# Optimization experiments

Hardware: AMD Instinct MI355X
Metric: run time of the kernel (lower is better)

## Reference

```python
import jax, jax.numpy as jnp
import numpy as np

B, N, D = 8, 1024, 768
H = 12
HD = D // H


def setup_inputs() -> dict:
    key = jax.random.key(0)
    ks = jax.random.split(key, 9)
    s = 1.0 / np.sqrt(D)
    return {
        "x": jax.random.normal(ks[0], (B, N, D), dtype=jnp.float32),
        "Wq": jax.random.normal(ks[1], (D, D), dtype=jnp.float32) * s,
        "bq": jax.random.normal(ks[2], (D,), dtype=jnp.float32) * 0.02,
        "Wk": jax.random.normal(ks[3], (D, D), dtype=jnp.float32) * s,
        "bk": jax.random.normal(ks[4], (D,), dtype=jnp.float32) * 0.02,
        "Wv": jax.random.normal(ks[5], (D, D), dtype=jnp.float32) * s,
        "bv": jax.random.normal(ks[6], (D,), dtype=jnp.float32) * 0.02,
        "Wo": jax.random.normal(ks[7], (D, D), dtype=jnp.float32) * s,
        "bo": jax.random.normal(ks[8], (D,), dtype=jnp.float32) * 0.02,
    }


def _softmax_one(x):
    # quiet softmax: exp(x - max) / (1 + sum exp(x - max))
    x = x - jnp.max(x, axis=-1, keepdims=True)
    ex = jnp.exp(x)
    return ex / (1.0 + jnp.sum(ex, axis=-1, keepdims=True))


def reference(x, Wq, bq, Wk, bk, Wv, bv, Wo, bo):
    q = x @ Wq + bq  # [B,N,D]
    k = x @ Wk + bk
    v = x @ Wv + bv
    # split heads -> [B,H,N,HD]
    qs = q.reshape(B, N, H, HD).transpose(0, 2, 1, 3)
    ks = k.reshape(B, N, H, HD).transpose(0, 2, 1, 3)
    vs = v.reshape(B, N, H, HD).transpose(0, 2, 1, 3)
    scores = jnp.einsum("bhqd,bhkd->bhqk", qs, ks) / np.sqrt(HD)
    attn = _softmax_one(scores)  # quiet_attention=True
    ctx = jnp.einsum("bhqk,bhkd->bhqd", attn, vs)
    ctx = ctx.transpose(0, 2, 1, 3).reshape(B, N, D)
    return ctx @ Wo + bo
```

## Files before the change

kernel.cpp:

```cpp
#include <hip/hip_runtime.h>
#include <cstdint>

#define DEV __device__ __forceinline__

typedef __bf16 bf16x4 __attribute__((ext_vector_type(4)));
typedef __bf16 bf16x8 __attribute__((ext_vector_type(8)));
typedef float  floatx4 __attribute__((ext_vector_type(4)));
typedef float  floatx16 __attribute__((ext_vector_type(16)));
typedef unsigned uint4v __attribute__((ext_vector_type(4)));

constexpr int BB = 8, NSEQ = 1024, DMODEL = 768, NH = 12, HD = 64;
constexpr int MTOK = BB * NSEQ;
constexpr int NQKV = 3 * DMODEL;
constexpr float CS = 0.18033688011112042f;

DEV void async_copy16(void* lds, const void* g) {
    __builtin_amdgcn_global_load_lds(
        (__attribute__((address_space(1))) void*)(const_cast<void*>(g)),
        (__attribute__((address_space(3))) void*)lds,
        16, 0, 0);
}

DEV floatx4 mfma16x32(bf16x8 a, bf16x8 b, floatx4 c) {
    return __builtin_amdgcn_mfma_f32_16x16x32_bf16(a, b, c, 0, 0, 0);
}
DEV floatx16 mfma32x16(bf16x8 a, bf16x8 b, floatx16 c) {
    return __builtin_amdgcn_mfma_f32_32x32x16_bf16(a, b, c, 0, 0, 0);
}
DEV unsigned cvtpk(float a, float b) {
    unsigned r;
    asm("v_cvt_pk_bf16_f32 %0, %1, %2" : "=v"(r) : "v"(a), "v"(b));
    return r;
}
DEV void swap32(unsigned& x, unsigned& y) {
    asm("v_permlane32_swap_b32 %0, %1" : "+v"(x), "+v"(y));
}


__global__ __launch_bounds__(256) void k_prep(const float* __restrict__ x,
                                              __bf16* __restrict__ xb,
                                              const float* __restrict__ Wq,
                                              const float* __restrict__ Wk,
                                              const float* __restrict__ Wv,
                                              const float* __restrict__ Wo,
                                              __bf16* __restrict__ wtqkv,
                                              __bf16* __restrict__ wto,
                                              const float* __restrict__ bq,
                                              const float* __restrict__ bk,
                                              const float* __restrict__ bv,
                                              float* __restrict__ bqkv) {
    __shared__ float tile[32][33];
    int bid = blockIdx.x, t = threadIdx.x;
    if (bid < 6144) {
        int i = (bid * 256 + t) * 4;
        float4 v = *(const float4*)(x + i);
        bf16x4 o;
        o[0] = (__bf16)v.x; o[1] = (__bf16)v.y; o[2] = (__bf16)v.z; o[3] = (__bf16)v.w;
        *(bf16x4*)(xb + i) = o;
    } else if (bid < 8448) {
        int idx = bid - 6144;
        int z = idx / 576, rem = idx % 576;
        int k0 = (rem % 24) * 32, n0 = (rem / 24) * 32;
        const float* W = (z == 0) ? Wq : (z == 1) ? Wk : (z == 2) ? Wv : Wo;
        int tx = t & 31, ty = t >> 5;
#pragma unroll
        for (int p = 0; p < 4; p++)
            tile[ty + 8 * p][tx] = W[(size_t)(k0 + ty + 8 * p) * 768 + n0 + tx];
        __syncthreads();
        __bf16* out = (z < 3) ? (wtqkv + (size_t)z * 768 * 768) : wto;
#pragma unroll
        for (int p = 0; p < 4; p++)
            out[(size_t)(n0 + ty + 8 * p) * 768 + k0 + tx] = (__bf16)tile[tx][ty + 8 * p];
    } else {
        int i = (bid - 8448) * 256 + t;
        if (i < 768) bqkv[i] = bq[i];
        else if (i < 1536) bqkv[i] = bk[i - 768];
        else bqkv[i] = bv[i - 1536];
    }
}

__global__ __launch_bounds__(256) void k_qkv(const __bf16* __restrict__ A,
                                             const __bf16* __restrict__ Bt,
                                             const float* __restrict__ bias,
                                             __bf16* __restrict__ qfb,
                                             __bf16* __restrict__ kfb,
                                             __bf16* __restrict__ vfb) {
    constexpr int SLOT = 16384;
    __shared__ __align__(16) __bf16 lds[2 * SLOT];
    int t = threadIdx.x, lane = t & 63, w = t >> 6;
    int quad = lane >> 4, n16 = lane & 15;
    int wm = w & 1, wn = w >> 1;
    int m0 = blockIdx.x * 128, n0 = blockIdx.y * 128;
    floatx4 acc[4][4] = {};

    auto stage_tile = [&](__bf16* slot, int k0) {
        __bf16* As_ = slot;
        __bf16* Bs_ = slot + 8192;
#pragma unroll
        for (int i = 0; i < 4; i++) {
            int off = t + i * 256;
            int row = off >> 3, pc = off & 7;
            int c = pc ^ (row & 7);
            async_copy16(&As_[row * 64 + pc * 8],
                         &A[(size_t)(m0 + row) * 768 + k0 + c * 8]);
        }
#pragma unroll
        for (int i = 0; i < 4; i++) {
            int off = t + i * 256;
            int row = off >> 3, pc = off & 7;
            int c = pc ^ (row & 7);
            async_copy16(&Bs_[row * 64 + pc * 8],
                         &Bt[(size_t)(n0 + row) * 768 + k0 + c * 8]);
        }
    };

    stage_tile(lds, 0);

#pragma unroll
    for (int kt = 0; kt < 12; kt++) {
        __bf16* As_ = lds + (kt & 1) * SLOT;
        __bf16* Bs_ = As_ + 8192;

        if (kt + 1 < 12) stage_tile(lds + ((kt + 1) & 1) * SLOT, (kt + 1) * 64);
        __builtin_amdgcn_sched_barrier(0);
        if (kt + 1 < 12) {
            asm volatile("s_waitcnt vmcnt(8)\n\ts_barrier" ::: "memory");
        } else {
            asm volatile("s_waitcnt vmcnt(0)\n\ts_barrier" ::: "memory");
        }
        __builtin_amdgcn_sched_barrier(0);

#pragma unroll
        for (int kfi = 0; kfi < 2; kfi++) {
            bf16x8 a[4], bfr[4];
#pragma unroll
            for (int rt = 0; rt < 4; rt++) {
                int row = wm * 64 + rt * 16 + n16;
                a[rt] = *(const bf16x8*)&As_[row * 64 + ((quad + 4 * kfi) ^ (row & 7)) * 8];
            }
#pragma unroll
            for (int ct = 0; ct < 4; ct++) {
                int row = wn * 64 + ct * 16 + n16;
                bfr[ct] = *(const bf16x8*)&Bs_[row * 64 + ((quad + 4 * kfi) ^ (row & 7)) * 8];
            }
            __builtin_amdgcn_s_setprio(1);
#pragma unroll
            for (int rt = 0; rt < 4; rt++)
#pragma unroll
                for (int ct = 0; ct < 4; ct++)
                    acc[rt][ct] = mfma16x32(a[rt], bfr[ct], acc[rt][ct]);
            __builtin_amdgcn_s_setprio(0);
        }

        if (kt + 1 < 12) {
            __builtin_amdgcn_sched_barrier(0);
            asm volatile("s_barrier" ::: "memory");
            __builtin_amdgcn_sched_barrier(0);
        }
    }

    if (n0 >= 1536) {
#pragma unroll
        for (int ct = 0; ct < 4; ct++) {
            int col = n0 + wn * 64 + ct * 16 + n16;
            float bs = bias[col];
            int cz = col - 1536;
            int hh = cz >> 6, hd = cz & 63;
            int mg = hd >> 5, l5v = hd & 31;
#pragma unroll
            for (int rt = 0; rt < 4; rt++) {
                int row0 = m0 + wm * 64 + rt * 16 + quad * 4;
                int bb = row0 >> 10, key = row0 & 1023;
                int iw = key >> 7, w_ = (key >> 5) & 3, kc = (key >> 4) & 1;
                int b5v = (key >> 3) & 1, j0 = key & 7;
                bf16x4 pk;
#pragma unroll
                for (int r = 0; r < 4; r++) pk[r] = (__bf16)(acc[rt][ct][r] + bs);
                size_t idx = (((((size_t)(bb * 12 + hh) * 8 + iw) * 4 + w_) * 2 + kc) * 2 + mg) * 512
                             + (size_t)(b5v * 32 + l5v) * 8 + j0;
                *(bf16x4*)&vfb[idx] = pk;
            }
        }
    } else {
        __bf16* dst = (n0 < 768) ? qfb : kfb;
        float mult = (n0 < 768) ? CS : 1.0f;
        bool isQ = (n0 < 768);
        int cofs = isQ ? 0 : 768;
#pragma unroll
        for (int ct = 0; ct < 4; ct++) {
            int col = n0 + wn * 64 + ct * 16 + n16;
            float bs = bias[col];
            int cz = col - cofs;
            int hh = cz >> 6, hd = cz & 63;
            int kfi = hd >> 4, b5v = (hd >> 3) & 1, j = hd & 7;
#pragma unroll
            for (int rt = 0; rt < 4; rt++) {
                int row0 = m0 + wm * 64 + rt * 16 + quad * 4;
                int bb = row0 >> 10, q10 = row0 & 1023;
                size_t idx;
                if (isQ) {
                    int qt = q10 >> 5, l5v = q10 & 31;
                    idx = (((size_t)(bb * 12 + hh) * 32 + qt) * 4 + kfi) * 512
                          + (size_t)(b5v * 32 + l5v) * 8 + j;
                } else {
                    int iw = q10 >> 7, w_ = (q10 >> 5) & 3, l5v = q10 & 31;
                    idx = ((((size_t)(bb * 12 + hh) * 8 + iw) * 4 + w_) * 4 + kfi) * 512
                          + (size_t)(b5v * 32 + l5v) * 8 + j;
                }
#pragma unroll
                for (int r = 0; r < 4; r++)
                    dst[idx + (size_t)r * 8] = (__bf16)((acc[rt][ct][r] + bs) * mult);
            }
        }
    }
}

__global__ __launch_bounds__(256) void k_oproj(const __bf16* __restrict__ A,
                                               const __bf16* __restrict__ Bt,
                                               const float* __restrict__ bias,
                                               float* __restrict__ C) {
    constexpr int SLOT = 12288;
    __shared__ __align__(16) __bf16 lds[2 * SLOT];
    int t = threadIdx.x, lane = t & 63, w = t >> 6;
    int quad = lane >> 4, n16 = lane & 15;
    int wm = w & 1, wn = w >> 1;
    int m0 = blockIdx.x * 128, n0 = blockIdx.y * 64;
    floatx4 acc[4][2] = {};

    auto stage_tile = [&](__bf16* slot, int k0) {
        __bf16* As_ = slot;
        __bf16* Bs_ = slot + 8192;
#pragma unroll
        for (int i = 0; i < 4; i++) {
            int off = t + i * 256;
            int row = off >> 3, pc = off & 7;
            int c = pc ^ (row & 7);
            async_copy16(&As_[row * 64 + pc * 8],
                         &A[(size_t)(m0 + row) * 768 + k0 + c * 8]);
        }
#pragma unroll
        for (int i = 0; i < 2; i++) {
            int off = t + i * 256;
            int row = off >> 3, pc = off & 7;
            int c = pc ^ (row & 7);
            async_copy16(&Bs_[row * 64 + pc * 8],
                         &Bt[(size_t)(n0 + row) * 768 + k0 + c * 8]);
        }
    };

    stage_tile(lds, 0);

#pragma unroll
    for (int kt = 0; kt < 12; kt++) {
        __bf16* As_ = lds + (kt & 1) * SLOT;
        __bf16* Bs_ = As_ + 8192;

        if (kt + 1 < 12) stage_tile(lds + ((kt + 1) & 1) * SLOT, (kt + 1) * 64);
        __builtin_amdgcn_sched_barrier(0);
        if (kt + 1 < 12) {
            asm volatile("s_waitcnt vmcnt(6)\n\ts_barrier" ::: "memory");
        } else {
            asm volatile("s_waitcnt vmcnt(0)\n\ts_barrier" ::: "memory");
        }
        __builtin_amdgcn_sched_barrier(0);

#pragma unroll
        for (int kfi = 0; kfi < 2; kfi++) {
            bf16x8 a[4], bfr[2];
#pragma unroll
            for (int rt = 0; rt < 4; rt++) {
                int row = wm * 64 + rt * 16 + n16;
                a[rt] = *(const bf16x8*)&As_[row * 64 + ((quad + 4 * kfi) ^ (row & 7)) * 8];
            }
#pragma unroll
            for (int ct = 0; ct < 2; ct++) {
                int row = wn * 32 + ct * 16 + n16;
                bfr[ct] = *(const bf16x8*)&Bs_[row * 64 + ((quad + 4 * kfi) ^ (row & 7)) * 8];
            }
            __builtin_amdgcn_s_setprio(1);
#pragma unroll
            for (int rt = 0; rt < 4; rt++)
#pragma unroll
                for (int ct = 0; ct < 2; ct++)
                    acc[rt][ct] = mfma16x32(a[rt], bfr[ct], acc[rt][ct]);
            __builtin_amdgcn_s_setprio(0);
        }

        if (kt + 1 < 12) {
            __builtin_amdgcn_sched_barrier(0);
            asm volatile("s_barrier" ::: "memory");
            __builtin_amdgcn_sched_barrier(0);
        }
    }

#pragma unroll
    for (int ct = 0; ct < 2; ct++) {
        int col = n0 + wn * 32 + ct * 16 + n16;
        float bs = bias[col];
#pragma unroll
        for (int rt = 0; rt < 4; rt++) {
#pragma unroll
            for (int r = 0; r < 4; r++) {
                int row = m0 + wm * 64 + rt * 16 + quad * 4 + r;
                C[(size_t)row * DMODEL + col] = acc[rt][ct][r] + bs;
            }
        }
    }
}

__global__ __launch_bounds__(256) void k_attn(const __bf16* __restrict__ QF,
                                              const __bf16* __restrict__ KF,
                                              const __bf16* __restrict__ VF,
                                              __bf16* __restrict__ ctx) {
    __shared__ __align__(16) unsigned char smem[18432];
    float* buf0 = (float*)smem;
    float* buf1 = (float*)(smem + 8704);
    float* Lsum = (float*)(smem + 17408);
    float* Pmax = (float*)(smem + 17920);

    int t = threadIdx.x, lane = t & 63, w = t >> 6;
    int l5 = lane & 31, b5 = lane >> 5;
    int id = blockIdx.x;
    int bB = id & 7;
    int seq = id >> 3;
    int h = seq % 12;
    int qt = seq / 12;
    int q0 = qt * 32;
    int bh = bB * NH + h;

    bf16x8 qf[4];
    {
        const __bf16* qp = QF + ((size_t)(bh * 32 + qt) * 4) * 512 + lane * 8;
#pragma unroll
        for (int kfi = 0; kfi < 4; kfi++)
            qf[kfi] = *(const bf16x8*)(qp + kfi * 512);
    }
    const __bf16* kp = KF + ((size_t)(bh * 8) * 4 + w) * 2048 + lane * 8;
    const __bf16* vp = VF + ((size_t)(bh * 8) * 4 + w) * 2048 + lane * 8;

    floatx16 acc[2] = {};
    float rs = 0.f, pm = 0.f;

    auto compute = [&](bf16x8 (&kf)[4], bf16x8 (&vf)[4]) {
        floatx16 s = {};
#pragma unroll
        for (int kfi = 0; kfi < 4; kfi++)
            s = mfma32x16(kf[kfi], qf[kfi], s);
        float p[16];
#pragma unroll
        for (int r = 0; r < 16; r++) {
            p[r] = __builtin_amdgcn_exp2f(s[r]);
            rs += p[r];
            pm = fmaxf(pm, p[r]);
        }
        unsigned x0 = cvtpk(p[0], p[1]),   y0 = cvtpk(p[4], p[5]);
        unsigned x1 = cvtpk(p[2], p[3]),   y1 = cvtpk(p[6], p[7]);
        unsigned x2 = cvtpk(p[8], p[9]),   y2 = cvtpk(p[12], p[13]);
        unsigned x3 = cvtpk(p[10], p[11]), y3 = cvtpk(p[14], p[15]);
        swap32(x0, y0); swap32(x1, y1); swap32(x2, y2); swap32(x3, y3);
        uint4v pa = {x0, x1, y0, y1};
        uint4v pbv = {x2, x3, y2, y3};
        bf16x8 P0 = __builtin_bit_cast(bf16x8, pa);
        bf16x8 P1 = __builtin_bit_cast(bf16x8, pbv);
        acc[0] = mfma32x16(vf[0], P0, acc[0]);
        acc[1] = mfma32x16(vf[1], P0, acc[1]);
        acc[0] = mfma32x16(vf[2], P1, acc[0]);
        acc[1] = mfma32x16(vf[3], P1, acc[1]);
    };

    bf16x8 ka[4], kb[4], vv[4];
#pragma unroll
    for (int f = 0; f < 4; f++) ka[f] = *(const bf16x8*)(kp + f * 512);
    kp += 8192;

    for (int i = 0; i < 8; i += 2) {
#pragma unroll
        for (int f = 0; f < 4; f++) kb[f] = *(const bf16x8*)(kp + f * 512);
        kp += 8192;
#pragma unroll
        for (int f = 0; f < 4; f++) vv[f] = *(const bf16x8*)(vp + f * 512);
        vp += 8192;
        compute(ka, vv);
        if (i < 6) {
#pragma unroll
            for (int f = 0; f < 4; f++) ka[f] = *(const bf16x8*)(kp + f * 512);
            kp += 8192;
        }
#pragma unroll
        for (int f = 0; f < 4; f++) vv[f] = *(const bf16x8*)(vp + f * 512);
        vp += 8192;
        compute(kb, vv);
    }

    rs += __shfl_xor(rs, 32);
    pm = fmaxf(pm, __shfl_xor(pm, 32));
    if (lane < 32) {
        Lsum[w * 32 + lane] = rs;
        Pmax[w * 32 + lane] = pm;
    }

    float* mybuf = (w & 1) ? buf1 : buf0;
    if (w < 2) {
#pragma unroll
        for (int mg = 0; mg < 2; mg++)
#pragma unroll
            for (int rq = 0; rq < 4; rq++) {
                floatx4 v = {acc[mg][rq * 4 + 0], acc[mg][rq * 4 + 1],
                             acc[mg][rq * 4 + 2], acc[mg][rq * 4 + 3]};
                *(floatx4*)&mybuf[l5 * 68 + mg * 32 + b5 * 4 + rq * 8] = v;
            }
    }
    __syncthreads();
    if (w >= 2) {
#pragma unroll
        for (int mg = 0; mg < 2; mg++)
#pragma unroll
            for (int rq = 0; rq < 4; rq++) {
                float* p = &mybuf[l5 * 68 + mg * 32 + b5 * 4 + rq * 8];
                floatx4 cur = *(const floatx4*)p;
                floatx4 v = {acc[mg][rq * 4 + 0], acc[mg][rq * 4 + 1],
                             acc[mg][rq * 4 + 2], acc[mg][rq * 4 + 3]};
                *(floatx4*)p = cur + v;
            }
    }
    __syncthreads();

    int qrow = t >> 3;
    int hh = (t & 7) * 8;
    float l = Lsum[qrow] + Lsum[32 + qrow] + Lsum[64 + qrow] + Lsum[96 + qrow];
    float pmx = fmaxf(fmaxf(Pmax[qrow], Pmax[32 + qrow]),
                      fmaxf(Pmax[64 + qrow], Pmax[96 + qrow]));
    float invd = 1.f / (pmx + l);
    floatx4 v0 = *(const floatx4*)&buf0[qrow * 68 + hh];
    floatx4 v1 = *(const floatx4*)&buf0[qrow * 68 + hh + 4];
    floatx4 u0 = *(const floatx4*)&buf1[qrow * 68 + hh];
    floatx4 u1 = *(const floatx4*)&buf1[qrow * 68 + hh + 4];
    bf16x8 o;
#pragma unroll
    for (int j = 0; j < 4; j++) o[j] = (__bf16)((v0[j] + u0[j]) * invd);
#pragma unroll
    for (int j = 0; j < 4; j++) o[j + 4] = (__bf16)((v1[j] + u1[j]) * invd);
    __bf16* dst = ctx + (size_t)(bB * NSEQ + q0 + qrow) * DMODEL + h * 64 + hh;
    *(bf16x8*)dst = o;
}

extern "C" void kernel_launch(void* const* d_in, const int* in_sizes, int n_in,
                              void* d_out, int out_size, void* d_ws, size_t ws_size,
                              hipStream_t stream) {
    (void)in_sizes; (void)n_in; (void)out_size;
    const float* x  = (const float*)d_in[0];
    const float* Wq = (const float*)d_in[1];
    const float* bq = (const float*)d_in[2];
    const float* Wk = (const float*)d_in[3];
    const float* bk = (const float*)d_in[4];
    const float* Wv = (const float*)d_in[5];
    const float* bv = (const float*)d_in[6];
    const float* Wo = (const float*)d_in[7];
    const float* bo = (const float*)d_in[8];
    float* out = (float*)d_out;

    char* ws = (char*)d_ws;
    size_t off = 0;
    auto alloc = [&](size_t bytes) {
        void* p = ws + off;
        off += (bytes + 255) & ~(size_t)255;
        return p;
    };
    __bf16* xb    = (__bf16*)alloc((size_t)MTOK * DMODEL * 2);
    __bf16* wtqkv = (__bf16*)alloc((size_t)NQKV * DMODEL * 2);
    __bf16* wto   = (__bf16*)alloc((size_t)DMODEL * DMODEL * 2);
    float*  bqkv  = (float*)alloc((size_t)NQKV * 4);
    __bf16* qfb   = (__bf16*)alloc((size_t)MTOK * DMODEL * 2);
    __bf16* kfb   = (__bf16*)alloc((size_t)MTOK * DMODEL * 2);
    __bf16* vfb   = (__bf16*)alloc((size_t)MTOK * DMODEL * 2);
    if (off > ws_size) return;
    __bf16* ctx = xb;

    k_prep<<<dim3(8457), dim3(256), 0, stream>>>(x, xb, Wq, Wk, Wv, Wo, wtqkv, wto,
                                                 bq, bk, bv, bqkv);
    k_qkv<<<dim3(64, 18), dim3(256), 0, stream>>>(xb, wtqkv, bqkv, qfb, kfb, vfb);
    k_attn<<<dim3(3072), dim3(256), 0, stream>>>(qfb, kfb, vfb, ctx);
    k_oproj<<<dim3(64, 12), dim3(256), 0, stream>>>(ctx, wto, bo, out);
}
```

Before: 183.1 us.

## Give each attention wave its own query tile over full key range, drop LDS reduction

```diff
diff --git a/kernel.cpp b/kernel.cpp
--- a/kernel.cpp
+++ b/kernel.cpp
@@ -5,6 +5,7 @@
 
 typedef __bf16 bf16x4 __attribute__((ext_vector_type(4)));
 typedef __bf16 bf16x8 __attribute__((ext_vector_type(8)));
+typedef float  floatx2 __attribute__((ext_vector_type(2)));
 typedef float  floatx4 __attribute__((ext_vector_type(4)));
 typedef float  floatx16 __attribute__((ext_vector_type(16)));
 typedef unsigned uint4v __attribute__((ext_vector_type(4)));
@@ -312,20 +313,14 @@
                                               const __bf16* __restrict__ KF,
                                               const __bf16* __restrict__ VF,
                                               __bf16* __restrict__ ctx) {
-    __shared__ __align__(16) unsigned char smem[18432];
-    float* buf0 = (float*)smem;
-    float* buf1 = (float*)(smem + 8704);
-    float* Lsum = (float*)(smem + 17408);
-    float* Pmax = (float*)(smem + 17920);
-
     int t = threadIdx.x, lane = t & 63, w = t >> 6;
     int l5 = lane & 31, b5 = lane >> 5;
     int id = blockIdx.x;
     int bB = id & 7;
     int seq = id >> 3;
     int h = seq % 12;
-    int qt = seq / 12;
-    int q0 = qt * 32;
+    int qb = seq / 12;
+    int qt = qb * 4 + w;
     int bh = bB * NH + h;
 
     bf16x8 qf[4];
@@ -335,11 +330,12 @@
         for (int kfi = 0; kfi < 4; kfi++)
             qf[kfi] = *(const bf16x8*)(qp + kfi * 512);
     }
-    const __bf16* kp = KF + ((size_t)(bh * 8) * 4 + w) * 2048 + lane * 8;
-    const __bf16* vp = VF + ((size_t)(bh * 8) * 4 + w) * 2048 + lane * 8;
+    const __bf16* kp = KF + (size_t)(bh * 32) * 2048 + lane * 8;
+    const __bf16* vp = VF + (size_t)(bh * 32) * 2048 + lane * 8;
 
     floatx16 acc[2] = {};
-    float rs = 0.f, pm = 0.f;
+    floatx2 rs2 = {0.f, 0.f};
+    float pm = 0.f;
 
     auto compute = [&](bf16x8 (&kf)[4], bf16x8 (&vf)[4]) {
         floatx16 s = {};
@@ -348,10 +344,13 @@
             s = mfma32x16(kf[kfi], qf[kfi], s);
         float p[16];
 #pragma unroll
-        for (int r = 0; r < 16; r++) {
+        for (int r = 0; r < 16; r++)
             p[r] = __builtin_amdgcn_exp2f(s[r]);
-            rs += p[r];
-            pm = fmaxf(pm, p[r]);
+#pragma unroll
+        for (int r = 0; r < 16; r += 2) {
+            floatx2 pp = {p[r], p[r + 1]};
+            rs2 += pp;
+            pm = fmaxf(fmaxf(p[r], p[r + 1]), pm);
         }
         unsigned x0 = cvtpk(p[0], p[1]),   y0 = cvtpk(p[4], p[5]);
         unsigned x1 = cvtpk(p[2], p[3]),   y1 = cvtpk(p[6], p[7]);
@@ -371,77 +370,43 @@
     bf16x8 ka[4], kb[4], vv[4];
 #pragma unroll
     for (int f = 0; f < 4; f++) ka[f] = *(const bf16x8*)(kp + f * 512);
-    kp += 8192;
-
-    for (int i = 0; i < 8; i += 2) {
+    kp += 2048;
+
+    for (int c = 0; c < 32; c += 2) {
 #pragma unroll
         for (int f = 0; f < 4; f++) kb[f] = *(const bf16x8*)(kp + f * 512);
-        kp += 8192;
+        kp += 2048;
 #pragma unroll
         for (int f = 0; f < 4; f++) vv[f] = *(const bf16x8*)(vp + f * 512);
-        vp += 8192;
+        vp += 2048;
         compute(ka, vv);
-        if (i < 6) {
+        if (c < 30) {
 #pragma unroll
             for (int f = 0; f < 4; f++) ka[f] = *(const bf16x8*)(kp + f * 512);
-            kp += 8192;
+            kp += 2048;
         }
 #pragma unroll
         for (int f = 0; f < 4; f++) vv[f] = *(const bf16x8*)(vp + f * 512);
-        vp += 8192;
+        vp += 2048;
         compute(kb, vv);
     }
 
+    float rs = rs2[0] + rs2[1];
     rs += __shfl_xor(rs, 32);
     pm = fmaxf(pm, __shfl_xor(pm, 32));
-    if (lane < 32) {
-        Lsum[w * 32 + lane] = rs;
-        Pmax[w * 32 + lane] = pm;
-    }
-
-    float* mybuf = (w & 1) ? buf1 : buf0;
-    if (w < 2) {
-#pragma unroll
-        for (int mg = 0; mg < 2; mg++)
-#pragma unroll
-            for (int rq = 0; rq < 4; rq++) {
-                floatx4 v = {acc[mg][rq * 4 + 0], acc[mg][rq * 4 + 1],
-                             acc[mg][rq * 4 + 2], acc[mg][rq * 4 + 3]};
-                *(floatx4*)&mybuf[l5 * 68 + mg * 32 + b5 * 4 + rq * 8] = v;
-            }
-    }
-    __syncthreads();
-    if (w >= 2) {
-#pragma unroll
-        for (int mg = 0; mg < 2; mg++)
-#pragma unroll
-            for (int rq = 0; rq < 4; rq++) {
-                float* p = &mybuf[l5 * 68 + mg * 32 + b5 * 4 + rq * 8];
-                floatx4 cur = *(const floatx4*)p;
-                floatx4 v = {acc[mg][rq * 4 + 0], acc[mg][rq * 4 + 1],
-                             acc[mg][rq * 4 + 2], acc[mg][rq * 4 + 3]};
-                *(floatx4*)p = cur + v;
-            }
-    }
-    __syncthreads();
-
-    int qrow = t >> 3;
-    int hh = (t & 7) * 8;
-    float l = Lsum[qrow] + Lsum[32 + qrow] + Lsum[64 + qrow] + Lsum[96 + qrow];
-    float pmx = fmaxf(fmaxf(Pmax[qrow], Pmax[32 + qrow]),
-                      fmaxf(Pmax[64 + qrow], Pmax[96 + qrow]));
-    float invd = 1.f / (pmx + l);
-    floatx4 v0 = *(const floatx4*)&buf0[qrow * 68 + hh];
-    floatx4 v1 = *(const floatx4*)&buf0[qrow * 68 + hh + 4];
-    floatx4 u0 = *(const floatx4*)&buf1[qrow * 68 + hh];
-    floatx4 u1 = *(const floatx4*)&buf1[qrow * 68 + hh + 4];
-    bf16x8 o;
-#pragma unroll
-    for (int j = 0; j < 4; j++) o[j] = (__bf16)((v0[j] + u0[j]) * invd);
-#pragma unroll
-    for (int j = 0; j < 4; j++) o[j + 4] = (__bf16)((v1[j] + u1[j]) * invd);
-    __bf16* dst = ctx + (size_t)(bB * NSEQ + q0 + qrow) * DMODEL + h * 64 + hh;
-    *(bf16x8*)dst = o;
+    float invd = 1.f / (pm + rs);
+
+    __bf16* dst = ctx + ((size_t)(bB * NSEQ) + qt * 32 + l5) * DMODEL + h * 64;
+#pragma unroll
+    for (int mg = 0; mg < 2; mg++)
+#pragma unroll
+        for (int rq = 0; rq < 4; rq++) {
+            bf16x4 o;
+#pragma unroll
+            for (int e = 0; e < 4; e++)
+                o[e] = (__bf16)(acc[mg][rq * 4 + e] * invd);
+            *(bf16x4*)(dst + mg * 32 + rq * 8 + b5 * 4) = o;
+        }
 }
 
 extern "C" void kernel_launch(void* const* d_in, const int* in_sizes, int n_in,
@@ -479,6 +444,6 @@
     k_prep<<<dim3(8457), dim3(256), 0, stream>>>(x, xb, Wq, Wk, Wv, Wo, wtqkv, wto,
                                                  bq, bk, bv, bqkv);
     k_qkv<<<dim3(64, 18), dim3(256), 0, stream>>>(xb, wtqkv, bqkv, qfb, kfb, vfb);
-    k_attn<<<dim3(3072), dim3(256), 0, stream>>>(qfb, kfb, vfb, ctx);
+    k_attn<<<dim3(768), dim3(256), 0, stream>>>(qfb, kfb, vfb, ctx);
     k_oproj<<<dim3(64, 12), dim3(256), 0, stream>>>(ctx, wto, bo, out);
 }
```

Measured after the change: 177.7 us. 1.03x faster.
